# Kernel optimization log

Measured on AMD Instinct MI355X. Metric: run time of the kernel, lower is better.

The kernel has to match this reference:

```python
import jax, jax.numpy as jnp
import numpy as np

NB_CLASSES = 10  # matches init_kwargs nb_classes


def setup_inputs() -> dict:
    key = jax.random.key(0)
    k1, k2 = jax.random.split(key)
    N, D = 500_000, 64
    h = jax.random.normal(k1, (N, D), dtype=jnp.float32)
    yhat = jax.random.randint(k2, (N,), 0, NB_CLASSES, dtype=jnp.int32)
    return {"h": h, "yhat": yhat}


def reference(h, yhat):
    # Original torch loop: for each class k, gather h_k = h[yhat==k],
    # M_k = mean_i(h_i h_i^T) * 0.5 + I, loss += 0.5 * logdet(M_k).
    # mean of outer products == (masked h)^T @ h / count_k, so we avoid
    # the ragged gather and any [N, D, D] intermediate entirely.
    N, D = h.shape
    eye = jnp.eye(D, dtype=h.dtype)

    def class_term(k):
        mask = (yhat == k).astype(h.dtype)            # [N]
        count = jnp.sum(mask)                         # B_k
        gram = jnp.einsum('nd,ne->de', mask[:, None] * h, h)  # sum_i h_i h_i^T
        M = gram * (0.5 / count) + eye                # [D, D], SPD
        _, logabsdet = jnp.linalg.slogdet(M)
        return 0.5 * logabsdet

    # NB_CLASSES is a small fixed constant -> Python loop is fine & keeps
    # peak memory at one extra [N, D] buffer.
    return jnp.sum(jnp.stack([class_term(k) for k in range(NB_CLASSES)]))
```

## Files before the change

### kernel.cpp

```cpp
#include <hip/hip_runtime.h>
#include <hip/hip_bf16.h>

typedef __attribute__((ext_vector_type(8))) short  short8;
typedef __attribute__((ext_vector_type(4))) float  f32x4;

#define NCLS 10
#define TILE 96
#define TPB  512
#define NQ   10
#define PPB  (NCLS * NQ * 256)
#define CH   16

#define AS1 __attribute__((address_space(1)))
#define AS3 __attribute__((address_space(3)))

#define MF(a, b, c) __builtin_amdgcn_mfma_f32_16x16x32_bf16((a), (b), (c), 0, 0, 0)

static __device__ inline unsigned short f2bf(float x) {
    unsigned u = __builtin_bit_cast(unsigned, x);
    return (unsigned short)((u + 0x7FFFu + ((u >> 16) & 1u)) >> 16);
}

static __device__ __forceinline__ void issue_tile(
        const float* __restrict__ h, const int* __restrict__ yhat,
        float* fsb, int* yb, long t, long N, int wid, int lane) {
#pragma unroll
    for (int i = 0; i < 3; ++i) {
        const int C = wid * 64 + i * 512 + lane;
        long row = t * TILE + (C >> 4);
        if (row > N - 1) row = N - 1;
        const float* gp = h + row * 64 + ((C & 15) << 2);
        __builtin_amdgcn_global_load_lds((const AS1 float*)gp,
                                         (AS3 float*)(fsb + (wid * 64 + i * 512) * 4),
                                         16, 0, 0);
    }
    if (wid == 0 && lane < 24) {
        long y0 = t * TILE + lane * 4;
        if (y0 > N - 4) y0 = N - 4;
        __builtin_amdgcn_global_load_lds((const AS1 int*)(yhat + y0),
                                         (AS3 int*)yb, 16, 0, 0);
    }
}

static __device__ __forceinline__ void compute_tile(
        const char* hsb, const unsigned short* mkb, int cls, int xcls, int wq,
        int hi, int col, f32x4 (&acc)[NQ], f32x4 (&accx)[3]) {
    const int sw = (col & 3) << 4;
#pragma unroll
    for (int ks = 0; ks < 3; ++ks) {
        const int b2 = ks * 64 + hi * 16;
        const short8 m = *(const short8*)((const char*)mkb + cls * 192 + b2);
        short8 raw[4], am[4];
#pragma unroll
        for (int nb = 0; nb < 4; ++nb) {
            raw[nb] = *(const short8*)(hsb + (nb * 16 + col) * 192 + (b2 ^ sw));
            am[nb]  = raw[nb] & m;
        }
        acc[0] = MF(am[0], am[0], acc[0]);
        acc[1] = MF(am[0], am[1], acc[1]);
        acc[2] = MF(am[0], am[2], acc[2]);
        acc[3] = MF(am[0], am[3], acc[3]);
        acc[4] = MF(am[1], am[1], acc[4]);
        acc[5] = MF(am[1], am[2], acc[5]);
        acc[6] = MF(am[1], am[3], acc[6]);
        acc[7] = MF(am[2], am[2], acc[7]);
        acc[8] = MF(am[2], am[3], acc[8]);
        acc[9] = MF(am[3], am[3], acc[9]);

        const short8 mx = *(const short8*)((const char*)mkb + xcls * 192 + b2);
        switch (wq) {
        case 0: { short8 x0 = raw[0] & mx, x1 = raw[1] & mx;
                  accx[0] = MF(x0, x0, accx[0]);
                  accx[1] = MF(x0, x1, accx[1]);
                  accx[2] = MF(x1, x1, accx[2]); } break;
        case 1: { short8 x0 = raw[0] & mx, x2 = raw[2] & mx, x3 = raw[3] & mx;
                  accx[0] = MF(x0, x2, accx[0]);
                  accx[1] = MF(x0, x3, accx[1]); } break;
        case 2: { short8 x1 = raw[1] & mx, x2 = raw[2] & mx, x3 = raw[3] & mx;
                  accx[0] = MF(x1, x2, accx[0]);
                  accx[1] = MF(x1, x3, accx[1]);
                  accx[2] = MF(x2, x2, accx[2]); } break;
        default:{ short8 x2 = raw[2] & mx, x3 = raw[3] & mx;
                  accx[0] = MF(x2, x3, accx[0]);
                  accx[1] = MF(x3, x3, accx[1]); } break;
        }
    }
}

__global__ __launch_bounds__(TPB, 4) void HL_gram(
        const float* __restrict__ h, const int* __restrict__ yhat,
        float* __restrict__ partials, int* __restrict__ cntp,
        long N, int ntiles, int G) {
    __shared__ __align__(16) float          fs[2][TILE * 64];
    __shared__ __align__(16) unsigned short hs[64 * TILE];
    __shared__ __align__(16) unsigned short mk[NCLS * TILE];
    __shared__ __align__(16) int            ylds[2][TILE];
    __shared__ int cntlds[16];

    const int tid  = threadIdx.x;
    const int wid  = tid >> 6;
    const int lane = tid & 63;
    const int hi   = lane >> 4;
    const int col  = lane & 15;

    const int cls  = wid;
    const int xcls = 8 + (wid >> 2);
    const int wq   = wid & 3;

    if (tid < 16) cntlds[tid] = 0;
    __syncthreads();

    f32x4 acc[NQ], accx[3];
#pragma unroll
    for (int q = 0; q < NQ; ++q) acc[q] = (f32x4){0.f, 0.f, 0.f, 0.f};
#pragma unroll
    for (int q = 0; q < 3; ++q)  accx[q] = (f32x4){0.f, 0.f, 0.f, 0.f};

    const int bid = blockIdx.x;
    const int K   = (ntiles - bid + G - 1) / G;

    issue_tile(h, yhat, &fs[0][0], &ylds[0][0], bid, N, wid, lane);
    if (K > 1)
        issue_tile(h, yhat, &fs[1][0], &ylds[1][0], bid + (long)G, N, wid, lane);

    for (int k = 0; k < K; ++k) {
        const long t  = bid + (long)k * G;
        const int  bk = k & 1;

        if (k + 1 < K) {
            if (wid == 0) asm volatile("s_waitcnt vmcnt(4)" ::: "memory");
            else          asm volatile("s_waitcnt vmcnt(3)" ::: "memory");
        } else {
            asm volatile("s_waitcnt vmcnt(0)" ::: "memory");
        }
        __builtin_amdgcn_s_barrier();

        if (tid < 384) {
            const int d  = lane;
            const int r0 = wid * 16;
            const float* fp = &fs[bk][0] + r0 * 64 + d;
            short8 w0, w1;
#pragma unroll
            for (int j = 0; j < 8; ++j) w0[j] = (short)f2bf(fp[j * 64]);
#pragma unroll
            for (int j = 0; j < 8; ++j) w1[j] = (short)f2bf(fp[(j + 8) * 64]);
            const int sw = (d & 3) << 4;
            char* hb = (char*)hs + d * 192;
            *(short8*)(hb + ((r0 * 2)      ^ sw)) = w0;
            *(short8*)(hb + ((r0 * 2 + 16) ^ sw)) = w1;
        } else {
            const int r = (wid - 6) * 64 + lane;
            if (r < TILE) {
                const long grow = t * TILE + r;
                const int y = (grow < N) ? ylds[bk][r] : -1;
#pragma unroll
                for (int c = 0; c < NCLS; ++c) {
                    mk[c * TILE + r] = (y == c) ? (unsigned short)0xFFFFu
                                                : (unsigned short)0u;
                    unsigned long long b = __ballot(y == c);
                    if (lane == 0) atomicAdd(&cntlds[c], __popcll(b));
                }
            }
        }

        asm volatile("s_waitcnt lgkmcnt(0)" ::: "memory");
        __builtin_amdgcn_s_barrier();

        if (k + 2 < K)
            issue_tile(h, yhat, &fs[bk][0], &ylds[bk][0],
                       bid + (long)(k + 2) * G, N, wid, lane);

        compute_tile((const char*)hs, mk, cls, xcls, wq, hi, col, acc, accx);
    }

    __syncthreads();

    float* pb = partials + (size_t)bid * PPB;
    {
        float* po = pb + (size_t)cls * (NQ * 256);
#pragma unroll
        for (int q = 0; q < NQ; ++q)
            *(f32x4*)(po + q * 256 + (lane << 2)) = acc[q];
    }
    {
        float* px = pb + (size_t)xcls * (NQ * 256) + (lane << 2);
        switch (wq) {
        case 0: *(f32x4*)(px + 0 * 256) = accx[0];
                *(f32x4*)(px + 1 * 256) = accx[1];
                *(f32x4*)(px + 4 * 256) = accx[2]; break;
        case 1: *(f32x4*)(px + 2 * 256) = accx[0];
                *(f32x4*)(px + 3 * 256) = accx[1]; break;
        case 2: *(f32x4*)(px + 5 * 256) = accx[0];
                *(f32x4*)(px + 6 * 256) = accx[1];
                *(f32x4*)(px + 7 * 256) = accx[2]; break;
        default:*(f32x4*)(px + 8 * 256) = accx[0];
                *(f32x4*)(px + 9 * 256) = accx[1]; break;
        }
    }
    if (tid < 16) cntp[bid * 16 + tid] = cntlds[tid];
}

__global__ void HL_reduce(const float* __restrict__ partials, float* __restrict__ rpart,
                          float* __restrict__ out, int G, int CS) {
    const int idx = blockIdx.x * blockDim.x + threadIdx.x;
    if (blockIdx.x == 0 && threadIdx.x == 0) out[0] = 0.f;
    if (idx >= CH * NCLS * NQ * 64) return;
    const int ch = idx / (NCLS * NQ * 64);
    const int r  = idx % (NCLS * NQ * 64);
    const int cq = r >> 6;
    const int l  = r & 63;

    int b0 = ch * CS;
    int b1 = b0 + CS; if (b1 > G) b1 = G;

    f32x4 s = (f32x4){0.f, 0.f, 0.f, 0.f};
    const float* p = partials + (size_t)cq * 256 + (l << 2);
    for (int b = b0; b < b1; ++b)
        s += *reinterpret_cast<const f32x4*>(p + (size_t)b * PPB);

    *reinterpret_cast<f32x4*>(rpart + ((size_t)ch * (NCLS * NQ) + cq) * 256 + (l << 2)) = s;
}

__global__ __launch_bounds__(64, 1) void HL_chol(
        const float* __restrict__ rpart, const int* __restrict__ cntp,
        float* __restrict__ out, int G) {
    __shared__ float M[64][68];
    __shared__ float lcol[64];
    const int cls = blockIdx.x;
    const int i   = threadIdx.x;

    int c = 0;
    for (int b = i; b < G; b += 64) c += cntp[b * 16 + cls];
#pragma unroll
    for (int off = 32; off > 0; off >>= 1) c += __shfl_xor(c, off);
    const float inv = 0.5f / (float)c;

    const int QMB[NQ] = {0,0,0,0,1,1,1,2,2,3};
    const int QNB[NQ] = {0,1,2,3,1,2,3,2,3,3};
    const float* rp = rpart + (size_t)cls * (NQ * 256);
#pragma unroll
    for (int q = 0; q < NQ; ++q) {
        f32x4 s = (f32x4){0.f, 0.f, 0.f, 0.f};
#pragma unroll
        for (int ch = 0; ch < CH; ++ch)
            s += *reinterpret_cast<const f32x4*>(rp + (size_t)ch * (NCLS * NQ * 256) + q * 256 + (i << 2));
        const int row0 = QMB[q] * 16 + ((i >> 4) << 2);
        const int colo = QNB[q] * 16 + (i & 15);
#pragma unroll
        for (int rr = 0; rr < 4; ++rr) {
            M[row0 + rr][colo] = s[rr];
            M[colo][row0 + rr] = s[rr];
        }
    }
    __syncthreads();

    float row[64];
#pragma unroll
    for (int c2 = 0; c2 < 64; ++c2)
        row[c2] = M[i][c2] * inv + (c2 == i ? 1.0f : 0.0f);

#pragma unroll
    for (int j = 0; j < 64; ++j) {
        const float piv = __shfl(row[j], j);
        const float li  = row[j] * rsqrtf(piv);
        lcol[i] = li;
        __syncthreads();
#pragma unroll
        for (int c2 = j + 1; c2 < 64; ++c2)
            row[c2] -= li * lcol[c2];
        __syncthreads();
    }

    float slog = 0.f;
#pragma unroll
    for (int j = 0; j < 64; ++j)
        if (i == j) slog = __logf(row[j]);
    slog += __shfl_down(slog, 32); slog += __shfl_down(slog, 16);
    slog += __shfl_down(slog, 8);  slog += __shfl_down(slog, 4);
    slog += __shfl_down(slog, 2);  slog += __shfl_down(slog, 1);
    if (i == 0) atomicAdd(out, 0.5f * slog);
}

extern "C" void kernel_launch(void* const* d_in, const int* in_sizes, int n_in,
                              void* d_out, int out_size, void* d_ws, size_t ws_size,
                              hipStream_t stream) {
    const float* h    = (const float*)d_in[0];
    const int*   yhat = (const int*)d_in[1];
    const long   N    = in_sizes[1];
    float* out = (float*)d_out;

    const size_t rpart_sz = (size_t)CH * NCLS * NQ * 256 * sizeof(float);
    const size_t cntp_off = rpart_sz;

    const int ntiles = (int)((N + TILE - 1) / TILE);
    int G = 512;
    {
        const size_t perG = 64 + (size_t)PPB * sizeof(float);
        if (ws_size > rpart_sz) {
            size_t maxG = (ws_size - rpart_sz) / perG;
            if ((size_t)G > maxG) G = (int)maxG;
        } else G = 1;
        if (G < 1) G = 1;
    }
    if (G > ntiles) G = ntiles;

    const size_t partials_off = cntp_off + (size_t)G * 16 * sizeof(int);
    float* rpart    = (float*)d_ws;
    int*   cntp     = (int*)((char*)d_ws + cntp_off);
    float* partials = (float*)((char*)d_ws + partials_off);

    HL_gram<<<G, TPB, 0, stream>>>(h, yhat, partials, cntp, N, ntiles, G);

    int CS = (G + CH - 1) / CH;
    const int rthreads = CH * NCLS * NQ * 64;
    HL_reduce<<<(rthreads + 255) / 256, 256, 0, stream>>>(partials, rpart, out, G, CS);

    HL_chol<<<NCLS, 64, 0, stream>>>(rpart, cntp, out, G);
}
```

Measured before the change: 91.83 us.

## Software-pipeline bf16 conversion with compute, shrink tile, store partials in fp16

Reduces the tile to 64 rows and triple-buffers the raw fp32 staging buffer while double-buffering the converted bf16 and mask buffers. This lets conversion of tile k overlap with MFMA compute of tile k-1 using a single barrier per iteration. Per-class counts move from LDS atomics to register ballot sums. Per-block partial Gram matrices are written as fp16 to halve workspace traffic for the reduce kernel, at some cost in accumulated precision and possible overflow or rounding in large partial sums.

```diff
diff --git a/kernel.cpp b/kernel.cpp
--- a/kernel.cpp
+++ b/kernel.cpp
@@ -1,11 +1,13 @@
 #include <hip/hip_runtime.h>
 #include <hip/hip_bf16.h>
 
-typedef __attribute__((ext_vector_type(8))) short  short8;
-typedef __attribute__((ext_vector_type(4))) float  f32x4;
+typedef __attribute__((ext_vector_type(8))) short    short8;
+typedef __attribute__((ext_vector_type(4))) float    f32x4;
+typedef __attribute__((ext_vector_type(4))) _Float16 f16x4;
+typedef __attribute__((ext_vector_type(2))) unsigned u32x2;
 
 #define NCLS 10
-#define TILE 96
+#define TILE 64
 #define TPB  512
 #define NQ   10
 #define PPB  (NCLS * NQ * 256)
@@ -16,25 +18,26 @@
 
 #define MF(a, b, c) __builtin_amdgcn_mfma_f32_16x16x32_bf16((a), (b), (c), 0, 0, 0)
 
-static __device__ inline unsigned short f2bf(float x) {
-    unsigned u = __builtin_bit_cast(unsigned, x);
-    return (unsigned short)((u + 0x7FFFu + ((u >> 16) & 1u)) >> 16);
+static __device__ __forceinline__ unsigned pkh2(float a, float b) {
+    unsigned short ha = __builtin_bit_cast(unsigned short, (_Float16)a);
+    unsigned short hb = __builtin_bit_cast(unsigned short, (_Float16)b);
+    return (unsigned)ha | ((unsigned)hb << 16);
 }
 
 static __device__ __forceinline__ void issue_tile(
         const float* __restrict__ h, const int* __restrict__ yhat,
         float* fsb, int* yb, long t, long N, int wid, int lane) {
 #pragma unroll
-    for (int i = 0; i < 3; ++i) {
-        const int C = wid * 64 + i * 512 + lane;
+    for (int i = 0; i < 2; ++i) {
+        const int C = (wid * 2 + i) * 64 + lane;
         long row = t * TILE + (C >> 4);
         if (row > N - 1) row = N - 1;
         const float* gp = h + row * 64 + ((C & 15) << 2);
         __builtin_amdgcn_global_load_lds((const AS1 float*)gp,
-                                         (AS3 float*)(fsb + (wid * 64 + i * 512) * 4),
+                                         (AS3 float*)(fsb + (wid * 2 + i) * 256),
                                          16, 0, 0);
     }
-    if (wid == 0 && lane < 24) {
+    if (wid == 0 && lane < 16) {
         long y0 = t * TILE + lane * 4;
         if (y0 > N - 4) y0 = N - 4;
         __builtin_amdgcn_global_load_lds((const AS1 int*)(yhat + y0),
@@ -43,17 +46,17 @@
 }
 
 static __device__ __forceinline__ void compute_tile(
-        const char* hsb, const unsigned short* mkb, int cls, int xcls, int wq,
+        const char* hsb, const char* mkb, int cls, int xcls, int wq,
         int hi, int col, f32x4 (&acc)[NQ], f32x4 (&accx)[3]) {
-    const int sw = (col & 3) << 4;
-#pragma unroll
-    for (int ks = 0; ks < 3; ++ks) {
+    const int sw = (col & 7) << 4;
+#pragma unroll
+    for (int ks = 0; ks < 2; ++ks) {
         const int b2 = ks * 64 + hi * 16;
-        const short8 m = *(const short8*)((const char*)mkb + cls * 192 + b2);
+        const short8 m = *(const short8*)(mkb + cls * 128 + b2);
         short8 raw[4], am[4];
 #pragma unroll
         for (int nb = 0; nb < 4; ++nb) {
-            raw[nb] = *(const short8*)(hsb + (nb * 16 + col) * 192 + (b2 ^ sw));
+            raw[nb] = *(const short8*)(hsb + (nb * 16 + col) * 128 + (b2 ^ sw));
             am[nb]  = raw[nb] & m;
         }
         acc[0] = MF(am[0], am[0], acc[0]);
@@ -67,7 +70,7 @@
         acc[8] = MF(am[2], am[3], acc[8]);
         acc[9] = MF(am[3], am[3], acc[9]);
 
-        const short8 mx = *(const short8*)((const char*)mkb + xcls * 192 + b2);
+        const short8 mx = *(const short8*)(mkb + xcls * 128 + b2);
         switch (wq) {
         case 0: { short8 x0 = raw[0] & mx, x1 = raw[1] & mx;
                   accx[0] = MF(x0, x0, accx[0]);
@@ -89,13 +92,12 @@
 
 __global__ __launch_bounds__(TPB, 4) void HL_gram(
         const float* __restrict__ h, const int* __restrict__ yhat,
-        float* __restrict__ partials, int* __restrict__ cntp,
+        _Float16* __restrict__ partials, int* __restrict__ cntp,
         long N, int ntiles, int G) {
-    __shared__ __align__(16) float          fs[2][TILE * 64];
-    __shared__ __align__(16) unsigned short hs[64 * TILE];
-    __shared__ __align__(16) unsigned short mk[NCLS * TILE];
-    __shared__ __align__(16) int            ylds[2][TILE];
-    __shared__ int cntlds[16];
+    __shared__ __align__(16) float          fs[3][TILE * 64];
+    __shared__ __align__(16) unsigned short hs[2][64 * TILE];
+    __shared__ __align__(16) unsigned short mk[2][NCLS * TILE];
+    __shared__ __align__(16) int            ylds[3][TILE];
 
     const int tid  = threadIdx.x;
     const int wid  = tid >> 6;
@@ -107,14 +109,12 @@
     const int xcls = 8 + (wid >> 2);
     const int wq   = wid & 3;
 
-    if (tid < 16) cntlds[tid] = 0;
-    __syncthreads();
-
     f32x4 acc[NQ], accx[3];
 #pragma unroll
     for (int q = 0; q < NQ; ++q) acc[q] = (f32x4){0.f, 0.f, 0.f, 0.f};
 #pragma unroll
     for (int q = 0; q < 3; ++q)  accx[q] = (f32x4){0.f, 0.f, 0.f, 0.f};
+    int c0=0,c1=0,c2=0,c3=0,c4=0,c5=0,c6=0,c7=0,c8=0,c9=0;
 
     const int bid = blockIdx.x;
     const int K   = (ntiles - bid + G - 1) / G;
@@ -125,82 +125,108 @@
 
     for (int k = 0; k < K; ++k) {
         const long t  = bid + (long)k * G;
-        const int  bk = k & 1;
+        const int  fk = k % 3;
+        const int  hk = k & 1;
 
         if (k + 1 < K) {
-            if (wid == 0) asm volatile("s_waitcnt vmcnt(4)" ::: "memory");
-            else          asm volatile("s_waitcnt vmcnt(3)" ::: "memory");
+            if (wid == 0) asm volatile("s_waitcnt vmcnt(3)" ::: "memory");
+            else          asm volatile("s_waitcnt vmcnt(2)" ::: "memory");
         } else {
             asm volatile("s_waitcnt vmcnt(0)" ::: "memory");
         }
-        __builtin_amdgcn_s_barrier();
-
-        if (tid < 384) {
-            const int d  = lane;
-            const int r0 = wid * 16;
-            const float* fp = &fs[bk][0] + r0 * 64 + d;
-            short8 w0, w1;
-#pragma unroll
-            for (int j = 0; j < 8; ++j) w0[j] = (short)f2bf(fp[j * 64]);
-#pragma unroll
-            for (int j = 0; j < 8; ++j) w1[j] = (short)f2bf(fp[(j + 8) * 64]);
-            const int sw = (d & 3) << 4;
-            char* hb = (char*)hs + d * 192;
-            *(short8*)(hb + ((r0 * 2)      ^ sw)) = w0;
-            *(short8*)(hb + ((r0 * 2 + 16) ^ sw)) = w1;
-        } else {
-            const int r = (wid - 6) * 64 + lane;
-            if (r < TILE) {
-                const long grow = t * TILE + r;
-                const int y = (grow < N) ? ylds[bk][r] : -1;
-#pragma unroll
-                for (int c = 0; c < NCLS; ++c) {
-                    mk[c * TILE + r] = (y == c) ? (unsigned short)0xFFFFu
-                                                : (unsigned short)0u;
-                    unsigned long long b = __ballot(y == c);
-                    if (lane == 0) atomicAdd(&cntlds[c], __popcll(b));
-                }
-            }
-        }
-
         asm volatile("s_waitcnt lgkmcnt(0)" ::: "memory");
         __builtin_amdgcn_s_barrier();
+        __builtin_amdgcn_sched_barrier(0);
+
+        {
+            const float* fp = &fs[fk][0] + (wid * 8) * 64 + lane;
+            float x[8];
+#pragma unroll
+            for (int j = 0; j < 8; ++j) x[j] = fp[j * 64];
+            u32x2 lohi[2];
+#pragma unroll
+            for (int p = 0; p < 4; ++p) {
+                __hip_bfloat162 pr = __float22bfloat162_rn(make_float2(x[2*p], x[2*p+1]));
+                unsigned u;
+                __builtin_memcpy(&u, &pr, 4);
+                ((unsigned*)lohi)[p] = u;
+            }
+            char* hb = (char*)&hs[hk][0] + lane * 128 + ((wid * 16) ^ ((lane & 7) << 4));
+            *(u32x2*)hb       = lohi[0];
+            *(u32x2*)(hb + 8) = lohi[1];
+        }
+        if (wid == 7) {
+            int y = ylds[fk][lane];
+            if (t * TILE + lane >= N) y = -1;
+            unsigned short* mb = &mk[hk][0];
+#pragma unroll
+            for (int c = 0; c < NCLS; ++c)
+                mb[c * TILE + lane] = (y == c) ? (unsigned short)0xFFFFu
+                                               : (unsigned short)0u;
+            c0 += (int)__popcll(__ballot(y == 0));
+            c1 += (int)__popcll(__ballot(y == 1));
+            c2 += (int)__popcll(__ballot(y == 2));
+            c3 += (int)__popcll(__ballot(y == 3));
+            c4 += (int)__popcll(__ballot(y == 4));
+            c5 += (int)__popcll(__ballot(y == 5));
+            c6 += (int)__popcll(__ballot(y == 6));
+            c7 += (int)__popcll(__ballot(y == 7));
+            c8 += (int)__popcll(__ballot(y == 8));
+            c9 += (int)__popcll(__ballot(y == 9));
+        }
 
         if (k + 2 < K)
-            issue_tile(h, yhat, &fs[bk][0], &ylds[bk][0],
+            issue_tile(h, yhat, &fs[(k + 2) % 3][0], &ylds[(k + 2) % 3][0],
                        bid + (long)(k + 2) * G, N, wid, lane);
 
-        compute_tile((const char*)hs, mk, cls, xcls, wq, hi, col, acc, accx);
-    }
-
-    __syncthreads();
-
-    float* pb = partials + (size_t)bid * PPB;
+        if (k > 0)
+            compute_tile((const char*)&hs[hk ^ 1][0], (const char*)&mk[hk ^ 1][0],
+                         cls, xcls, wq, hi, col, acc, accx);
+    }
+
+    asm volatile("s_waitcnt lgkmcnt(0)" ::: "memory");
+    __builtin_amdgcn_s_barrier();
+    __builtin_amdgcn_sched_barrier(0);
+    compute_tile((const char*)&hs[(K - 1) & 1][0], (const char*)&mk[(K - 1) & 1][0],
+                 cls, xcls, wq, hi, col, acc, accx);
+
+    _Float16* pb = partials + (size_t)bid * PPB;
     {
-        float* po = pb + (size_t)cls * (NQ * 256);
-#pragma unroll
-        for (int q = 0; q < NQ; ++q)
-            *(f32x4*)(po + q * 256 + (lane << 2)) = acc[q];
+        _Float16* po = pb + (size_t)cls * (NQ * 256);
+#pragma unroll
+        for (int q = 0; q < NQ; ++q) {
+            u32x2 pk; pk[0] = pkh2(acc[q][0], acc[q][1]);
+            pk[1] = pkh2(acc[q][2], acc[q][3]);
+            *(u32x2*)(po + q * 256 + (lane << 2)) = pk;
+        }
     }
     {
-        float* px = pb + (size_t)xcls * (NQ * 256) + (lane << 2);
+        _Float16* px = pb + (size_t)xcls * (NQ * 256) + (lane << 2);
+        u32x2 pk0, pk1, pk2;
+        pk0[0] = pkh2(accx[0][0], accx[0][1]); pk0[1] = pkh2(accx[0][2], accx[0][3]);
+        pk1[0] = pkh2(accx[1][0], accx[1][1]); pk1[1] = pkh2(accx[1][2], accx[1][3]);
+        pk2[0] = pkh2(accx[2][0], accx[2][1]); pk2[1] = pkh2(accx[2][2], accx[2][3]);
         switch (wq) {
-        case 0: *(f32x4*)(px + 0 * 256) = accx[0];
-                *(f32x4*)(px + 1 * 256) = accx[1];
-                *(f32x4*)(px + 4 * 256) = accx[2]; break;
-        case 1: *(f32x4*)(px + 2 * 256) = accx[0];
-                *(f32x4*)(px + 3 * 256) = accx[1]; break;
-        case 2: *(f32x4*)(px + 5 * 256) = accx[0];
-                *(f32x4*)(px + 6 * 256) = accx[1];
-                *(f32x4*)(px + 7 * 256) = accx[2]; break;
-        default:*(f32x4*)(px + 8 * 256) = accx[0];
-                *(f32x4*)(px + 9 * 256) = accx[1]; break;
-        }
-    }
-    if (tid < 16) cntp[bid * 16 + tid] = cntlds[tid];
-}
-
-__global__ void HL_reduce(const float* __restrict__ partials, float* __restrict__ rpart,
+        case 0: *(u32x2*)(px + 0 * 256) = pk0;
+                *(u32x2*)(px + 1 * 256) = pk1;
+                *(u32x2*)(px + 4 * 256) = pk2; break;
+        case 1: *(u32x2*)(px + 2 * 256) = pk0;
+                *(u32x2*)(px + 3 * 256) = pk1; break;
+        case 2: *(u32x2*)(px + 5 * 256) = pk0;
+                *(u32x2*)(px + 6 * 256) = pk1;
+                *(u32x2*)(px + 7 * 256) = pk2; break;
+        default:*(u32x2*)(px + 8 * 256) = pk0;
+                *(u32x2*)(px + 9 * 256) = pk1; break;
+        }
+    }
+    if (wid == 7 && lane == 0) {
+        int* cp = cntp + bid * 16;
+        cp[0]=c0; cp[1]=c1; cp[2]=c2; cp[3]=c3; cp[4]=c4;
+        cp[5]=c5; cp[6]=c6; cp[7]=c7; cp[8]=c8; cp[9]=c9;
+    }
+}
+
+__global__ void HL_reduce(const _Float16* __restrict__ partials, float* __restrict__ rpart,
                           float* __restrict__ out, int G, int CS) {
     const int idx = blockIdx.x * blockDim.x + threadIdx.x;
     if (blockIdx.x == 0 && threadIdx.x == 0) out[0] = 0.f;
@@ -214,10 +240,12 @@
     int b1 = b0 + CS; if (b1 > G) b1 = G;
 
     f32x4 s = (f32x4){0.f, 0.f, 0.f, 0.f};
-    const float* p = partials + (size_t)cq * 256 + (l << 2);
-    for (int b = b0; b < b1; ++b)
-        s += *reinterpret_cast<const f32x4*>(p + (size_t)b * PPB);
-
+    const _Float16* p = partials + (size_t)cq * 256 + (l << 2);
+    for (int b = b0; b < b1; ++b) {
+        f16x4 v = *(const f16x4*)(p + (size_t)b * PPB);
+        s[0] += (float)v[0]; s[1] += (float)v[1];
+        s[2] += (float)v[2]; s[3] += (float)v[3];
+    }
     *reinterpret_cast<f32x4*>(rpart + ((size_t)ch * (NCLS * NQ) + cq) * 256 + (l << 2)) = s;
 }
 
@@ -295,7 +323,7 @@
     const int ntiles = (int)((N + TILE - 1) / TILE);
     int G = 512;
     {
-        const size_t perG = 64 + (size_t)PPB * sizeof(float);
+        const size_t perG = 64 + (size_t)PPB * sizeof(_Float16);
         if (ws_size > rpart_sz) {
             size_t maxG = (ws_size - rpart_sz) / perG;
             if ((size_t)G > maxG) G = (int)maxG;
@@ -305,9 +333,9 @@
     if (G > ntiles) G = ntiles;
 
     const size_t partials_off = cntp_off + (size_t)G * 16 * sizeof(int);
-    float* rpart    = (float*)d_ws;
-    int*   cntp     = (int*)((char*)d_ws + cntp_off);
-    float* partials = (float*)((char*)d_ws + partials_off);
+    float*    rpart    = (float*)d_ws;
+    int*      cntp     = (int*)((char*)d_ws + cntp_off);
+    _Float16* partials = (_Float16*)((char*)d_ws + partials_off);
 
     HL_gram<<<G, TPB, 0, stream>>>(h, yhat, partials, cntp, N, ntiles, G);
 
```

After: 84.94 us. -7.5%, faster.
